# Kernel tuning notes

Hardware: AMD Instinct MI355X
Metric: run time of the kernel (lower is better)

## Reference

```python
import jax, jax.numpy as jnp
import numpy as np

EMBED_DIM = 768
NUM_HEADS = 12
HEAD_DIM = EMBED_DIM // NUM_HEADS
EPS = 1e-5  # nn.LayerNorm default


def setup_inputs() -> dict:
    key = jax.random.key(0)
    ks = jax.random.split(key, 7)
    D = EMBED_DIM
    s1 = 1.0 / np.sqrt(D)
    x = jax.random.normal(ks[0], (2, 2048, D), dtype=jnp.float32)
    # LayerNorm params
    gamma = jnp.ones((D,), jnp.float32)
    beta = jnp.zeros((D,), jnp.float32)
    # QKV projection (linear1): weight [3D, D], bias [3D]
    w1 = jax.random.uniform(ks[1], (3 * D, D), jnp.float32, -s1, s1)
    b1 = jax.random.uniform(ks[2], (3 * D,), jnp.float32, -s1, s1)
    # Output projection (linear2[0]): weight [D, D], bias [D]
    w2 = jax.random.uniform(ks[3], (D, D), jnp.float32, -s1, s1)
    b2 = jax.random.uniform(ks[4], (D,), jnp.float32, -s1, s1)
    return {"x": x, "gamma": gamma, "beta": beta, "w1": w1, "b1": b1, "w2": w2, "b2": b2}


def _layernorm(x, gamma, beta):
    mu = jnp.mean(x, axis=-1, keepdims=True)
    var = jnp.mean(jnp.square(x - mu), axis=-1, keepdims=True)
    return (x - mu) * jax.lax.rsqrt(var + EPS) * gamma + beta


def reference(x, gamma, beta, w1, b1, w2, b2) -> jnp.ndarray:
    B, L, D = x.shape
    H, Dh = NUM_HEADS, HEAD_DIM
    residual = x
    h = _layernorm(x, gamma, beta)
    qkv = h @ w1.T + b1  # [B, L, 3D]
    q, k, v = jnp.split(qkv, 3, axis=-1)
    # 'b n (h d) -> b h n d'
    q = q.reshape(B, L, H, Dh).transpose(0, 2, 1, 3)
    k = k.reshape(B, L, H, Dh).transpose(0, 2, 1, 3)
    v = v.reshape(B, L, H, Dh).transpose(0, 2, 1, 3)
    scores = jnp.einsum("bhqd,bhkd->bhqk", q, k) / jnp.sqrt(jnp.float32(Dh))
    attn = jax.nn.softmax(scores, axis=-1)  # dropout is identity in eval mode
    out = jnp.einsum("bhqk,bhkd->bhqd", attn, v)  # [B, H, L, Dh]
    out = out.transpose(0, 2, 1, 3).reshape(B, L, D)
    out = out @ w2.T + b2  # dropout identity in eval
    return residual + out
```

## Files before the change

kernel.cpp:

```cpp
#include <hip/hip_runtime.h>


#define DEV __device__ __forceinline__

typedef __attribute__((ext_vector_type(4))) float f32x4;
typedef __attribute__((ext_vector_type(8))) short s16x8;
typedef __attribute__((ext_vector_type(2))) int i32x2;

constexpr int Bb   = 2;
constexpr int Ll   = 2048;
constexpr int Dd   = 768;
constexpr int Hh   = 12;
constexpr int Dh   = 64;
constexpr int Mrows = Bb * Ll;
constexpr int N1   = 3 * Dd;

DEV unsigned short f2bf(float f) {
  union { float f; unsigned u; } v; v.f = f;
  unsigned r = v.u + 0x7fffu + ((v.u >> 16) & 1u);
  return (unsigned short)(r >> 16);
}

DEV void gload_lds16(const void* g, void* l) {
  __builtin_amdgcn_global_load_lds((const __attribute__((address_space(1))) unsigned int*)g,
                                   (__attribute__((address_space(3))) unsigned int*)l,
                                   16, 0, 0);
}

DEV f32x4 mfma16(s16x8 a, s16x8 b, f32x4 c) {
  return __builtin_amdgcn_mfma_f32_16x16x32_bf16(a, b, c, 0, 0, 0);
}

DEV float fexp2(float x) { float r; asm("v_exp_f32 %0, %1" : "=v"(r) : "v"(x)); return r; }
DEV float frcp(float x)  { float r; asm("v_rcp_f32 %0, %1" : "=v"(r) : "v"(x)); return r; }

DEV float redmax64(float x) {
  x = fmaxf(x, __shfl_xor(x, 16, 64));
  float a = x, b = x;
  asm volatile("v_permlane32_swap_b32 %0, %1" : "+v"(a), "+v"(b));
  return fmaxf(a, b);
}
DEV float redsum64(float x) {
  x += __shfl_xor(x, 16, 64);
  float a = x, b = x;
  asm volatile("v_permlane32_swap_b32 %0, %1" : "+v"(a), "+v"(b));
  return a + b;
}

DEV void ln_body(int row, int t, const float* __restrict__ x,
                 const float* __restrict__ gamma, const float* __restrict__ beta,
                 short* __restrict__ hbuf, float* red) {
  const float* xr = x + (size_t)row * Dd;
  float v0 = xr[t], v1 = xr[t + 256], v2 = xr[t + 512];
  float s = v0 + v1 + v2;
  float q = v0 * v0 + v1 * v1 + v2 * v2;
#pragma unroll
  for (int off = 32; off; off >>= 1) {
    s += __shfl_xor(s, off, 64);
    q += __shfl_xor(q, off, 64);
  }
  const int w = t >> 6, lane = t & 63;
  if (lane == 0) { red[w] = s; red[4 + w] = q; }
  __syncthreads();
  s = red[0] + red[1] + red[2] + red[3];
  q = red[4] + red[5] + red[6] + red[7];
  const float mean = s * (1.f / Dd);
  const float var  = q * (1.f / Dd) - mean * mean;
  const float rstd = rsqrtf(var + 1e-5f);
  short* hr = hbuf + (size_t)row * Dd;
  hr[t]       = (short)f2bf((v0 - mean) * rstd * gamma[t]       + beta[t]);
  hr[t + 256] = (short)f2bf((v1 - mean) * rstd * gamma[t + 256] + beta[t + 256]);
  hr[t + 512] = (short)f2bf((v2 - mean) * rstd * gamma[t + 512] + beta[t + 512]);
}

constexpr int W1E = N1 * Dd;
constexpr int W2E = Dd * Dd;

__global__ __launch_bounds__(256) void ln_kernel(const float* __restrict__ x,
                                                 const float* __restrict__ gamma,
                                                 const float* __restrict__ beta,
                                                 short* __restrict__ hbuf) {
  __shared__ float red[8];
  ln_body(blockIdx.x, threadIdx.x, x, gamma, beta, hbuf, red);
}

__global__ __launch_bounds__(256) void cvt_kernel(const float* __restrict__ w1,
                                                  const float* __restrict__ w2,
                                                  short* __restrict__ w1b,
                                                  short* __restrict__ w2b) {
  int i = blockIdx.x * 256 + threadIdx.x;
  const int stride = gridDim.x * 256;
  for (; i < W1E + W2E; i += stride) {
    if (i < W1E) w1b[i] = (short)f2bf(w1[i]);
    else         w2b[i - W1E] = (short)f2bf(w2[i - W1E]);
  }
}

__global__ __launch_bounds__(256) void prep_kernel(const float* __restrict__ x,
                                                   const float* __restrict__ gamma,
                                                   const float* __restrict__ beta,
                                                   short* __restrict__ hbuf,
                                                   const float* __restrict__ w1,
                                                   const float* __restrict__ w2,
                                                   short* __restrict__ w1b,
                                                   short* __restrict__ w2b) {
  __shared__ float red[8];
  if (blockIdx.x < (unsigned)Mrows) {
    ln_body(blockIdx.x, threadIdx.x, x, gamma, beta, hbuf, red);
  } else {
    int i = (blockIdx.x - Mrows) * 256 + threadIdx.x;
    for (; i < W1E + W2E; i += 1024 * 256) {
      if (i < W1E) w1b[i] = (short)f2bf(w1[i]);
      else         w2b[i - W1E] = (short)f2bf(w2[i - W1E]);
    }
  }
}

template <int EPI, int WSRC>
__global__ __launch_bounds__(256) void gemm_bt(const short* __restrict__ A,
                                               const void* __restrict__ Wp,
                                               const float* __restrict__ bias,
                                               const float* __restrict__ resid,
                                               void* __restrict__ outp,
                                               int N, int K) {
  __shared__ __align__(16) short As[2][128 * 64];
  __shared__ __align__(16) short Ws[2][128 * 64];
  const int tid  = threadIdx.x;
  const int lane = tid & 63, wid = tid >> 6;
  const int wr = wid >> 1, wc = wid & 1;
  const int g = lane >> 4, li = lane & 15;
  const int brow = blockIdx.y * 128, bcol = blockIdx.x * 128;

  f32x4 acc[4][4];
#pragma unroll
  for (int m = 0; m < 4; ++m)
#pragma unroll
    for (int n = 0; n < 4; ++n)
#pragma unroll
      for (int r = 0; r < 4; ++r) acc[m][n][r] = 0.f;

  if constexpr (WSRC == 0) {
    const short* W = (const short*)Wp;
    const int nt = K >> 6;
    auto stage = [&](int t, int buf) {
      const int ko = t << 6;
#pragma unroll
      for (int i = 0; i < 4; ++i) {
        const int idx = i * 256 + tid;
        const int r = idx >> 3, c = idx & 7;
        const int cs = c ^ (r & 7);
        gload_lds16(A + (size_t)(brow + r) * K + ko + cs * 8,
                    (char*)&As[buf][0] + idx * 16);
        gload_lds16(W + (size_t)(bcol + r) * K + ko + cs * 8,
                    (char*)&Ws[buf][0] + idx * 16);
      }
    };
    stage(0, 0);
    stage(1, 1);
    for (int it = 0; it < nt; ++it) {
      const int cur = it & 1;
      if (it + 1 < nt) asm volatile("s_waitcnt vmcnt(8)" ::: "memory");
      else             asm volatile("s_waitcnt vmcnt(0)" ::: "memory");
      __builtin_amdgcn_s_barrier();
      __builtin_amdgcn_sched_barrier(0);
#pragma unroll
      for (int kk = 0; kk < 2; ++kk) {
        s16x8 af[4], bf[4];
#pragma unroll
        for (int m = 0; m < 4; ++m) {
          const int row = wr * 64 + m * 16 + li;
          af[m] = *(const s16x8*)&As[cur][row * 64 + (((kk * 4 + g) ^ (li & 7)) & 7) * 8];
        }
#pragma unroll
        for (int n = 0; n < 4; ++n) {
          const int row = wc * 64 + n * 16 + li;
          bf[n] = *(const s16x8*)&Ws[cur][row * 64 + (((kk * 4 + g) ^ (li & 7)) & 7) * 8];
        }
#pragma unroll
        for (int m = 0; m < 4; ++m)
#pragma unroll
          for (int n = 0; n < 4; ++n)
            acc[m][n] = mfma16(af[m], bf[n], acc[m][n]);
      }
      __builtin_amdgcn_s_barrier();
      if (it + 2 < nt) stage(it + 2, cur);
    }
  } else {
    const float* W = (const float*)Wp;
    for (int kt = 0; kt < K; kt += 64) {
#pragma unroll
      for (int i = 0; i < 4; ++i) {
        const int idx = i * 256 + tid;
        const int r = idx >> 3, c = idx & 7;
        const int cs = c ^ (r & 7);
        gload_lds16(A + (size_t)(brow + r) * K + kt + cs * 8,
                    (char*)&As[0][0] + idx * 16);
      }
#pragma unroll
      for (int i = 0; i < 4; ++i) {
        const int idx = i * 256 + tid;
        const int r = idx >> 3, c = idx & 7;
        const float* wp = W + (size_t)(bcol + r) * K + kt + c * 8;
        const f32x4 lo = *(const f32x4*)wp;
        const f32x4 hi = *(const f32x4*)(wp + 4);
        s16x8 o;
#pragma unroll
        for (int j = 0; j < 4; ++j) {
          o[j]     = (short)f2bf(lo[j]);
          o[4 + j] = (short)f2bf(hi[j]);
        }
        *(s16x8*)((char*)&Ws[0][0] + (size_t)(r * 8 + (c ^ (r & 7))) * 16) = o;
      }
      __syncthreads();
#pragma unroll
      for (int kk = 0; kk < 2; ++kk) {
        s16x8 af[4], bf[4];
#pragma unroll
        for (int m = 0; m < 4; ++m) {
          const int row = wr * 64 + m * 16 + li;
          af[m] = *(const s16x8*)&As[0][row * 64 + (((kk * 4 + g) ^ (li & 7)) & 7) * 8];
        }
#pragma unroll
        for (int n = 0; n < 4; ++n) {
          const int row = wc * 64 + n * 16 + li;
          bf[n] = *(const s16x8*)&Ws[0][row * 64 + (((kk * 4 + g) ^ (li & 7)) & 7) * 8];
        }
#pragma unroll
        for (int m = 0; m < 4; ++m)
#pragma unroll
          for (int n = 0; n < 4; ++n)
            acc[m][n] = mfma16(af[m], bf[n], acc[m][n]);
      }
      __syncthreads();
    }
  }

#pragma unroll
  for (int m = 0; m < 4; ++m) {
#pragma unroll
    for (int n = 0; n < 4; ++n) {
      const int col = bcol + wc * 64 + n * 16 + li;
      const float bv = bias[col];
#pragma unroll
      for (int r = 0; r < 4; ++r) {
        const int row = brow + wr * 64 + m * 16 + g * 4 + r;
        const float v = acc[m][n][r] + bv;
        if (EPI == 0) {
          ((short*)outp)[(size_t)row * N + col] = (short)f2bf(v);
        } else {
          const size_t o = (size_t)row * N + col;
          ((float*)outp)[o] = v + resid[o];
        }
      }
    }
  }
}

#define TRRD(dst, addr, OFF)                                                   \
  asm volatile("ds_read_b64_tr_b16 %0, %1 offset:" #OFF                        \
               : "=v"(dst) : "v"(addr))

__global__ __launch_bounds__(256) void attn_kernel(const short* __restrict__ qkv,
                                                   short* __restrict__ obuf) {
  __shared__ __align__(16) short Ks[2][64 * 64];
  __shared__ __align__(16) short Vt[2][64 * 64];
  __shared__ __align__(16) short Ps[4][16 * 64];
  const int tid  = threadIdx.x;
  const int lane = tid & 63, w = tid >> 6;
  const int g = lane >> 4, li = lane & 15;
  const int bh = blockIdx.y;
  const int b = bh / Hh, h = bh % Hh;
  const size_t rowbase = (size_t)b * Ll * N1;
  const int q0 = blockIdx.x * 64 + w * 16;
  constexpr float kScale = 0.125f * 1.44269504f;
  constexpr float kThrRaw = 8.f / kScale;
  constexpr int KVSTRIDE = 64 * N1;

  s16x8 qf[2];
#pragma unroll
  for (int ks = 0; ks < 2; ++ks)
    qf[ks] = *(const s16x8*)(qkv + rowbase + (size_t)(q0 + li) * N1 +
                             h * Dh + ks * 32 + g * 8);

  f32x4 oa[4];
  float m_ = -1e30f, l_ = 0.f;
#pragma unroll
  for (int dn = 0; dn < 4; ++dn)
#pragma unroll
    for (int r = 0; r < 4; ++r) oa[dn][r] = 0.f;

  constexpr int NT = Ll / 64;

  const int ia = tid, ib = 256 + tid;
  const int ra = ia >> 3, ca = ia & 7, rb = ib >> 3, cb = ib & 7;
  const short* kpa = qkv + rowbase + Dd + h * Dh + (size_t)ra * N1 + (ca ^ (ra & 7)) * 8;
  const short* kpb = qkv + rowbase + Dd + h * Dh + (size_t)rb * N1 + (cb ^ (rb & 7)) * 8;
  const int Ta = ia >> 3, Tb = ib >> 3;
  const short* vpa = qkv + rowbase + 2 * Dd + h * Dh +
                     (size_t)((Ta & 15) * 4 + (ca >> 1)) * N1 + (Ta >> 4) * 16 + (ia & 1) * 8;
  const short* vpb = qkv + rowbase + 2 * Dd + h * Dh +
                     (size_t)((Tb & 15) * 4 + (cb >> 1)) * N1 + (Tb >> 4) * 16 + (ib & 1) * 8;
  char* KsB = (char*)&Ks[0][0];
  char* VtB = (char*)&Vt[0][0];
  const int dsta = ia * 16, dstb = ib * 16;

  int koff[4][2];
#pragma unroll
  for (int n = 0; n < 4; ++n) {
    koff[n][0] = ((n * 16 + li) * 64 + ((g ^ (li & 7)) & 7) * 8) * 2;
    koff[n][1] = ((n * 16 + li) * 64 + (((4 + g) ^ (li & 7)) & 7) * 8) * 2;
  }
  int pwoff[4], proff[2];
#pragma unroll
  for (int n = 0; n < 4; ++n)
    pwoff[n] = li * 128 + (((2 * n + (g >> 1)) ^ (li & 7)) << 4) + 8 * (g & 1);
#pragma unroll
  for (int kk = 0; kk < 2; ++kk)
    proff[kk] = li * 128 + (((4 * kk + g) ^ (li & 7)) << 4);
  char* Pw = (char*)&Ps[w][0];
  const unsigned vlane = (unsigned)((lane >> 4) * 256 + (lane & 15) * 2);
  const unsigned vbase0 = (unsigned)(unsigned long long)(&Vt[0][0]) + vlane;

  auto stage = [&](int buf) {
    const int bo = buf << 13;
    gload_lds16(kpa, KsB + bo + dsta);
    gload_lds16(kpb, KsB + bo + dstb);
    gload_lds16(vpa, VtB + bo + dsta);
    gload_lds16(vpb, VtB + bo + dstb);
    kpa += KVSTRIDE; kpb += KVSTRIDE; vpa += KVSTRIDE; vpb += KVSTRIDE;
  };

  stage(0);
  stage(1);

  for (int kt = 0; kt < NT; ++kt) {
    const int cur = kt & 1;
    const int curo = cur << 13;
    if (kt + 1 < NT) asm volatile("s_waitcnt vmcnt(4)" ::: "memory");
    else             asm volatile("s_waitcnt vmcnt(0)" ::: "memory");
    __builtin_amdgcn_s_barrier();
    __builtin_amdgcn_sched_barrier(0);

    f32x4 s[4];
    __builtin_amdgcn_s_setprio(1);
#pragma unroll
    for (int n = 0; n < 4; ++n) {
      s16x8 kf0 = *(const s16x8*)(KsB + curo + koff[n][0]);
      s16x8 kf1 = *(const s16x8*)(KsB + curo + koff[n][1]);
      f32x4 z;
#pragma unroll
      for (int r = 0; r < 4; ++r) z[r] = 0.f;
      z = mfma16(kf0, qf[0], z);
      z = mfma16(kf1, qf[1], z);
      s[n] = z;
    }
    __builtin_amdgcn_s_setprio(0);

    const float l0 = fmaxf(fmaxf(s[0][0], s[0][1]), s[0][2]);
    const float l1 = fmaxf(fmaxf(s[0][3], s[1][0]), s[1][1]);
    const float l2 = fmaxf(fmaxf(s[1][2], s[1][3]), s[2][0]);
    const float l3 = fmaxf(fmaxf(s[2][1], s[2][2]), s[2][3]);
    const float l4 = fmaxf(fmaxf(s[3][0], s[3][1]), s[3][2]);
    float mx = fmaxf(fmaxf(fmaxf(fmaxf(l0, l1), l2), fmaxf(l3, l4)), s[3][3]);
    mx = redmax64(mx);
    if (!__all(mx - m_ <= kThrRaw)) {
      const float mnew = fmaxf(m_, mx);
      const float sc = fexp2((m_ - mnew) * kScale);
      float scq[4];
#pragma unroll
      for (int r = 0; r < 4; ++r)
        scq[r] = __shfl(sc, (lane & 48) + ((lane & 48) >> 2) + r, 64);
#pragma unroll
      for (int dn = 0; dn < 4; ++dn)
#pragma unroll
        for (int r = 0; r < 4; ++r) oa[dn][r] *= scq[r];
      l_ *= sc;
      m_ = mnew;
    }
    const float msc = m_ * kScale;
    float rs = 0.f;
#pragma unroll
    for (int n = 0; n < 4; ++n)
#pragma unroll
      for (int r = 0; r < 4; ++r) {
        const float p = fexp2(fmaf(s[n][r], kScale, -msc));
        s[n][r] = p;
        rs += p;
      }
    rs = redsum64(rs);
    l_ += rs;

#pragma unroll
    for (int n = 0; n < 4; ++n) {
      unsigned u0, u1;
      asm("v_cvt_pk_bf16_f32 %0, %1, %2" : "=v"(u0) : "v"(s[n][0]), "v"(s[n][1]));
      asm("v_cvt_pk_bf16_f32 %0, %1, %2" : "=v"(u1) : "v"(s[n][2]), "v"(s[n][3]));
      i32x2 pv; pv[0] = (int)u0; pv[1] = (int)u1;
      *(i32x2*)(Pw + pwoff[n]) = pv;
    }

    s16x8 pf[2];
#pragma unroll
    for (int kk = 0; kk < 2; ++kk)
      pf[kk] = *(const s16x8*)(Pw + proff[kk]);

    union VU { long l[2]; s16x8 v; };
    VU vu[4][2];
    {
      const unsigned vaddr = vbase0 + (unsigned)curo;
      TRRD(vu[0][0].l[0], vaddr, 0);    TRRD(vu[0][0].l[1], vaddr, 128);
      TRRD(vu[0][1].l[0], vaddr, 1024); TRRD(vu[0][1].l[1], vaddr, 1152);
      TRRD(vu[1][0].l[0], vaddr, 2048); TRRD(vu[1][0].l[1], vaddr, 2176);
      TRRD(vu[1][1].l[0], vaddr, 3072); TRRD(vu[1][1].l[1], vaddr, 3200);
      TRRD(vu[2][0].l[0], vaddr, 4096); TRRD(vu[2][0].l[1], vaddr, 4224);
      TRRD(vu[2][1].l[0], vaddr, 5120); TRRD(vu[2][1].l[1], vaddr, 5248);
      TRRD(vu[3][0].l[0], vaddr, 6144); TRRD(vu[3][0].l[1], vaddr, 6272);
      TRRD(vu[3][1].l[0], vaddr, 7168); TRRD(vu[3][1].l[1], vaddr, 7296);
    }
    asm volatile("s_waitcnt lgkmcnt(0)" ::: "memory");
    __builtin_amdgcn_sched_barrier(0);

    __builtin_amdgcn_s_setprio(1);
#pragma unroll
    for (int dn = 0; dn < 4; ++dn) {
      oa[dn] = mfma16(pf[0], vu[dn][0].v, oa[dn]);
      oa[dn] = mfma16(pf[1], vu[dn][1].v, oa[dn]);
    }
    __builtin_amdgcn_s_setprio(0);

    __builtin_amdgcn_s_barrier();
    if (kt + 2 < NT) stage(cur);
  }

  {
#pragma unroll
    for (int r = 0; r < 4; ++r) {
      const float lq = __shfl(l_, (lane & 48) + ((lane & 48) >> 2) + r, 64);
      const float inv = frcp(lq);
      const int row = b * Ll + q0 + g * 4 + r;
#pragma unroll
      for (int dn = 0; dn < 4; ++dn)
        obuf[(size_t)row * Dd + h * Dh + dn * 16 + li] =
            (short)f2bf(oa[dn][r] * inv);
    }
  }
}

extern "C" void kernel_launch(void* const* d_in, const int* in_sizes, int n_in,
                              void* d_out, int out_size, void* d_ws, size_t ws_size,
                              hipStream_t stream) {
  const float* x     = (const float*)d_in[0];
  const float* gamma = (const float*)d_in[1];
  const float* beta  = (const float*)d_in[2];
  const float* w1    = (const float*)d_in[3];
  const float* b1    = (const float*)d_in[4];
  const float* w2    = (const float*)d_in[5];
  const float* b2    = (const float*)d_in[6];
  float* out = (float*)d_out;
  char* ws = (char*)d_ws;

  if (ws_size >= 29884416) {
    short* qkvb = (short*)(ws);
    short* hb   = (short*)(ws + 18874368);
    short* w1b  = (short*)(ws + 25165824);
    short* w2b  = (short*)(ws + 28704768);
    prep_kernel<<<dim3(Mrows + 1024), dim3(256), 0, stream>>>(
        x, gamma, beta, hb, w1, w2, w1b, w2b);
    gemm_bt<0, 0><<<dim3(N1 / 128, Mrows / 128), dim3(256), 0, stream>>>(
        hb, w1b, b1, nullptr, (void*)qkvb, N1, Dd);
    attn_kernel<<<dim3(Ll / 64, Bb * Hh), dim3(256), 0, stream>>>(qkvb, hb);
    gemm_bt<1, 0><<<dim3(Dd / 128, Mrows / 128), dim3(256), 0, stream>>>(
        hb, w2b, b2, x, (void*)out, Dd, Dd);
  } else if (ws_size >= 17301504) {
    short* qkvb = (short*)(ws);
    short* hb   = (short*)(ws + 9437184);
    short* w1b  = (short*)(ws + 12582912);
    short* w2b  = (short*)(ws + 16121856);
    cvt_kernel<<<dim3(1024), dim3(256), 0, stream>>>(w1, w2, w1b, w2b);
    for (int b = 0; b < Bb; ++b) {
      const size_t ro = (size_t)b * Ll * Dd;
      ln_kernel<<<dim3(Ll), dim3(256), 0, stream>>>(x + ro, gamma, beta, hb);
      gemm_bt<0, 0><<<dim3(N1 / 128, Ll / 128), dim3(256), 0, stream>>>(
          hb, w1b, b1, nullptr, (void*)qkvb, N1, Dd);
      attn_kernel<<<dim3(Ll / 64, Hh), dim3(256), 0, stream>>>(qkvb, hb);
      gemm_bt<1, 0><<<dim3(Dd / 128, Ll / 128), dim3(256), 0, stream>>>(
          hb, w2b, b2, x + ro, (void*)(out + ro), Dd, Dd);
    }
  } else {
    short* qkvb = (short*)(ws);
    short* hb   = (short*)(ws + 9437184);
    for (int b = 0; b < Bb; ++b) {
      const size_t ro = (size_t)b * Ll * Dd;
      ln_kernel<<<dim3(Ll), dim3(256), 0, stream>>>(x + ro, gamma, beta, hb);
      gemm_bt<0, 1><<<dim3(N1 / 128, Ll / 128), dim3(256), 0, stream>>>(
          hb, w1, b1, nullptr, (void*)qkvb, N1, Dd);
      attn_kernel<<<dim3(Ll / 64, Hh), dim3(256), 0, stream>>>(qkvb, hb);
      gemm_bt<1, 1><<<dim3(Dd / 128, Ll / 128), dim3(256), 0, stream>>>(
          hb, w2, b2, x + ro, (void*)(out + ro), Dd, Dd);
    }
  }
}
```

Before: 116.4 us.

## Software-pipeline QK^T one tile ahead in attention and add XCD-aware block swizzle

The attention loop now computes the QK^T scores for the next KV tile while the softmax and PV work for the current tile proceeds. K and V staging are split into separate lambdas so the next K tile can be issued early and V later, and the vmcnt waits are adjusted to match. Separately, an XCD-aware remap of workgroup IDs is added to both the GEMM and attention kernels so that neighbouring tiles land on the same XCD for L2 reuse. In exchange the kernel holds more registers for the extra score buffer and has more complex wait/barrier ordering, which risks lower occupancy or hazards on the K buffer.

```diff
diff --git a/kernel.cpp b/kernel.cpp
--- a/kernel.cpp
+++ b/kernel.cpp
@@ -116,6 +116,11 @@
   }
 }
 
+DEV unsigned xcd_swz(unsigned f, unsigned nwg) {
+  if ((nwg & 7u) != 0u) return f;
+  return (f & 7u) * (nwg >> 3) + (f >> 3);
+}
+
 template <int EPI, int WSRC>
 __global__ __launch_bounds__(256) void gemm_bt(const short* __restrict__ A,
                                                const void* __restrict__ Wp,
@@ -129,7 +134,9 @@
   const int lane = tid & 63, wid = tid >> 6;
   const int wr = wid >> 1, wc = wid & 1;
   const int g = lane >> 4, li = lane & 15;
-  const int brow = blockIdx.y * 128, bcol = blockIdx.x * 128;
+  const unsigned o = xcd_swz(blockIdx.y * gridDim.x + blockIdx.x,
+                             gridDim.x * gridDim.y);
+  const int brow = (int)(o / gridDim.x) * 128, bcol = (int)(o % gridDim.x) * 128;
 
   f32x4 acc[4][4];
 #pragma unroll
@@ -203,13 +210,13 @@
         const float* wp = W + (size_t)(bcol + r) * K + kt + c * 8;
         const f32x4 lo = *(const f32x4*)wp;
         const f32x4 hi = *(const f32x4*)(wp + 4);
-        s16x8 o;
+        s16x8 oo;
 #pragma unroll
         for (int j = 0; j < 4; ++j) {
-          o[j]     = (short)f2bf(lo[j]);
-          o[4 + j] = (short)f2bf(hi[j]);
+          oo[j]     = (short)f2bf(lo[j]);
+          oo[4 + j] = (short)f2bf(hi[j]);
         }
-        *(s16x8*)((char*)&Ws[0][0] + (size_t)(r * 8 + (c ^ (r & 7))) * 16) = o;
+        *(s16x8*)((char*)&Ws[0][0] + (size_t)(r * 8 + (c ^ (r & 7))) * 16) = oo;
       }
       __syncthreads();
 #pragma unroll
@@ -248,8 +255,8 @@
         if (EPI == 0) {
           ((short*)outp)[(size_t)row * N + col] = (short)f2bf(v);
         } else {
-          const size_t o = (size_t)row * N + col;
-          ((float*)outp)[o] = v + resid[o];
+          const size_t o2 = (size_t)row * N + col;
+          ((float*)outp)[o2] = v + resid[o2];
         }
       }
     }
@@ -268,10 +275,11 @@
   const int tid  = threadIdx.x;
   const int lane = tid & 63, w = tid >> 6;
   const int g = lane >> 4, li = lane & 15;
-  const int bh = blockIdx.y;
+  const unsigned o = xcd_swz(blockIdx.y * 32u + blockIdx.x, gridDim.x * gridDim.y);
+  const int bh = (int)(o >> 5);
   const int b = bh / Hh, h = bh % Hh;
   const size_t rowbase = (size_t)b * Ll * N1;
-  const int q0 = blockIdx.x * 64 + w * 16;
+  const int q0 = (int)(o & 31u) * 64 + w * 16;
   constexpr float kScale = 0.125f * 1.44269504f;
   constexpr float kThrRaw = 8.f / kScale;
   constexpr int KVSTRIDE = 64 * N1;
@@ -321,47 +329,70 @@
   const unsigned vlane = (unsigned)((lane >> 4) * 256 + (lane & 15) * 2);
   const unsigned vbase0 = (unsigned)(unsigned long long)(&Vt[0][0]) + vlane;
 
-  auto stage = [&](int buf) {
+  auto stageK = [&](int buf) {
     const int bo = buf << 13;
     gload_lds16(kpa, KsB + bo + dsta);
     gload_lds16(kpb, KsB + bo + dstb);
+    kpa += KVSTRIDE; kpb += KVSTRIDE;
+  };
+  auto stageV = [&](int buf) {
+    const int bo = buf << 13;
     gload_lds16(vpa, VtB + bo + dsta);
     gload_lds16(vpb, VtB + bo + dstb);
-    kpa += KVSTRIDE; kpb += KVSTRIDE; vpa += KVSTRIDE; vpb += KVSTRIDE;
+    vpa += KVSTRIDE; vpb += KVSTRIDE;
   };
 
-  stage(0);
-  stage(1);
+  stageK(0); stageV(0); stageK(1); stageV(1);
+  asm volatile("s_waitcnt vmcnt(4)" ::: "memory");
+  __builtin_amdgcn_s_barrier();
+  __builtin_amdgcn_sched_barrier(0);
+
+  f32x4 zA[4], zB[4];
+#pragma unroll
+  for (int n = 0; n < 4; ++n) {
+    s16x8 kf0 = *(const s16x8*)(KsB + koff[n][0]);
+    s16x8 kf1 = *(const s16x8*)(KsB + koff[n][1]);
+    f32x4 z;
+#pragma unroll
+    for (int r = 0; r < 4; ++r) z[r] = 0.f;
+    z = mfma16(kf0, qf[0], z);
+    z = mfma16(kf1, qf[1], z);
+    zA[n] = z;
+  }
 
   for (int kt = 0; kt < NT; ++kt) {
     const int cur = kt & 1;
     const int curo = cur << 13;
-    if (kt + 1 < NT) asm volatile("s_waitcnt vmcnt(4)" ::: "memory");
+    const int nxto = (cur ^ 1) << 13;
+    if (kt + 1 < NT) asm volatile("s_waitcnt vmcnt(2)" ::: "memory");
     else             asm volatile("s_waitcnt vmcnt(0)" ::: "memory");
     __builtin_amdgcn_s_barrier();
     __builtin_amdgcn_sched_barrier(0);
 
-    f32x4 s[4];
-    __builtin_amdgcn_s_setprio(1);
-#pragma unroll
-    for (int n = 0; n < 4; ++n) {
-      s16x8 kf0 = *(const s16x8*)(KsB + curo + koff[n][0]);
-      s16x8 kf1 = *(const s16x8*)(KsB + curo + koff[n][1]);
-      f32x4 z;
-#pragma unroll
-      for (int r = 0; r < 4; ++r) z[r] = 0.f;
-      z = mfma16(kf0, qf[0], z);
-      z = mfma16(kf1, qf[1], z);
-      s[n] = z;
-    }
-    __builtin_amdgcn_s_setprio(0);
-
-    const float l0 = fmaxf(fmaxf(s[0][0], s[0][1]), s[0][2]);
-    const float l1 = fmaxf(fmaxf(s[0][3], s[1][0]), s[1][1]);
-    const float l2 = fmaxf(fmaxf(s[1][2], s[1][3]), s[2][0]);
-    const float l3 = fmaxf(fmaxf(s[2][1], s[2][2]), s[2][3]);
-    const float l4 = fmaxf(fmaxf(s[3][0], s[3][1]), s[3][2]);
-    float mx = fmaxf(fmaxf(fmaxf(fmaxf(l0, l1), l2), fmaxf(l3, l4)), s[3][3]);
+    if (kt + 2 < NT) stageK(cur);
+
+    if (kt + 1 < NT) {
+      __builtin_amdgcn_s_setprio(1);
+#pragma unroll
+      for (int n = 0; n < 4; ++n) {
+        s16x8 kf0 = *(const s16x8*)(KsB + nxto + koff[n][0]);
+        s16x8 kf1 = *(const s16x8*)(KsB + nxto + koff[n][1]);
+        f32x4 z;
+#pragma unroll
+        for (int r = 0; r < 4; ++r) z[r] = 0.f;
+        z = mfma16(kf0, qf[0], z);
+        z = mfma16(kf1, qf[1], z);
+        zB[n] = z;
+      }
+      __builtin_amdgcn_s_setprio(0);
+    }
+
+    const float l0 = fmaxf(fmaxf(zA[0][0], zA[0][1]), zA[0][2]);
+    const float l1 = fmaxf(fmaxf(zA[0][3], zA[1][0]), zA[1][1]);
+    const float l2 = fmaxf(fmaxf(zA[1][2], zA[1][3]), zA[2][0]);
+    const float l3 = fmaxf(fmaxf(zA[2][1], zA[2][2]), zA[2][3]);
+    const float l4 = fmaxf(fmaxf(zA[3][0], zA[3][1]), zA[3][2]);
+    float mx = fmaxf(fmaxf(fmaxf(fmaxf(l0, l1), l2), fmaxf(l3, l4)), zA[3][3]);
     mx = redmax64(mx);
     if (!__all(mx - m_ <= kThrRaw)) {
       const float mnew = fmaxf(m_, mx);
@@ -383,8 +414,8 @@
     for (int n = 0; n < 4; ++n)
 #pragma unroll
       for (int r = 0; r < 4; ++r) {
-        const float p = fexp2(fmaf(s[n][r], kScale, -msc));
-        s[n][r] = p;
+        const float p = fexp2(fmaf(zA[n][r], kScale, -msc));
+        zA[n][r] = p;
         rs += p;
       }
     rs = redsum64(rs);
@@ -393,8 +424,8 @@
 #pragma unroll
     for (int n = 0; n < 4; ++n) {
       unsigned u0, u1;
-      asm("v_cvt_pk_bf16_f32 %0, %1, %2" : "=v"(u0) : "v"(s[n][0]), "v"(s[n][1]));
-      asm("v_cvt_pk_bf16_f32 %0, %1, %2" : "=v"(u1) : "v"(s[n][2]), "v"(s[n][3]));
+      asm("v_cvt_pk_bf16_f32 %0, %1, %2" : "=v"(u0) : "v"(zA[n][0]), "v"(zA[n][1]));
+      asm("v_cvt_pk_bf16_f32 %0, %1, %2" : "=v"(u1) : "v"(zA[n][2]), "v"(zA[n][3]));
       i32x2 pv; pv[0] = (int)u0; pv[1] = (int)u1;
       *(i32x2*)(Pw + pwoff[n]) = pv;
     }
@@ -429,7 +460,11 @@
     __builtin_amdgcn_s_setprio(0);
 
     __builtin_amdgcn_s_barrier();
-    if (kt + 2 < NT) stage(cur);
+    if (kt + 2 < NT) stageV(cur);
+    if (kt + 1 < NT) {
+#pragma unroll
+      for (int n = 0; n < 4; ++n) zA[n] = zB[n];
+    }
   }
 
   {
```

New measurement: 114.2 us. No clear change (-1.9%).
